# Kernel optimization log

Hardware: AMD Instinct MI355X
Metric: run time of the kernel (lower is better)

The kernel has to match this reference:

```python
import jax, jax.numpy as jnp
import numpy as np
import math

N_NODES = 10000
N_EDGES = 30000
N_FEAT = 128
N_GRAPHS = 50
HEADS = 8
OUT_DIM = 10


def _lin_params(key, fin, fout):
    kw, kb = jax.random.split(key)
    s = 1.0 / math.sqrt(fin)
    w = jax.random.uniform(kw, (fin, fout), jnp.float32, -s, s)
    b = jax.random.uniform(kb, (fout,), jnp.float32, -s, s)
    return w, b


def setup_inputs() -> dict:
    key = jax.random.key(0)
    ks = jax.random.split(key, 20)
    inp = {}
    inp["x"] = jax.random.normal(ks[0], (N_NODES, N_FEAT), jnp.float32)
    inp["edge_index"] = jax.random.randint(ks[1], (2, N_EDGES), 0, N_NODES)
    inp["batch"] = jnp.sort(jax.random.randint(ks[2], (N_NODES,), 0, N_GRAPHS))
    # (fin, out_channels) per layer; internal width = out_channels * HEADS
    dims = [(128, 512), (512, 256), (256, 64)]
    ki = 3
    for i, (fin, cout) in enumerate(dims, 1):
        hc = cout * HEADS
        inp[f"q{i}_w"], inp[f"q{i}_b"] = _lin_params(ks[ki], fin, hc); ki += 1
        inp[f"k{i}_w"], inp[f"k{i}_b"] = _lin_params(ks[ki], fin, hc); ki += 1
        inp[f"v{i}_w"], inp[f"v{i}_b"] = _lin_params(ks[ki], fin, hc); ki += 1
        inp[f"s{i}_w"], inp[f"s{i}_b"] = _lin_params(ks[ki], fin, cout); ki += 1
    inp["gate_w"], inp["gate_b"] = _lin_params(ks[ki], 64, 1); ki += 1
    inp["fc_w"], inp["fc_b"] = _lin_params(ks[ki], 64, OUT_DIM)
    return inp


def _tconv(x, src, dst, qw, qb, kw_, kb_, vw, vb, sw, sb):
    # PyG TransformerConv, heads=HEADS, concat=False (mean over heads), root_weight=True
    N = x.shape[0]
    hc = qw.shape[1]
    C = hc // HEADS
    q = (x @ qw + qb).reshape(N, HEADS, C)
    k = (x @ kw_ + kb_).reshape(N, HEADS, C)
    v = (x @ vw + vb).reshape(N, HEADS, C)
    # per-edge attention logits [E, H]
    alpha = (q[dst] * k[src]).sum(-1) * (1.0 / math.sqrt(C))
    # segment softmax over incoming edges of each destination node
    m = jax.ops.segment_max(alpha, dst, num_segments=N)
    ex = jnp.exp(alpha - m[dst])
    den = jax.ops.segment_sum(ex, dst, num_segments=N)
    w = ex / jnp.maximum(den[dst], 1e-16)
    agg = jax.ops.segment_sum(w[:, :, None] * v[src], dst, num_segments=N)  # [N,H,C]
    return agg.mean(axis=1) + x @ sw + sb


def reference(x, edge_index, batch,
              q1_w, q1_b, k1_w, k1_b, v1_w, v1_b, s1_w, s1_b,
              q2_w, q2_b, k2_w, k2_b, v2_w, v2_b, s2_w, s2_b,
              q3_w, q3_b, k3_w, k3_b, v3_w, v3_b, s3_w, s3_b,
              gate_w, gate_b, fc_w, fc_b):
    src, dst = edge_index[0], edge_index[1]
    h = jax.nn.elu(_tconv(x, src, dst, q1_w, q1_b, k1_w, k1_b, v1_w, v1_b, s1_w, s1_b))
    h = jax.nn.elu(_tconv(h, src, dst, q2_w, q2_b, k2_w, k2_b, v2_w, v2_b, s2_w, s2_b))
    h = jax.nn.elu(_tconv(h, src, dst, q3_w, q3_b, k3_w, k3_b, v3_w, v3_b, s3_w, s3_b))
    # GlobalAttention pooling: softmax(gate) within each graph, weighted sum
    gate = h @ gate_w + gate_b  # [N,1]
    gm = jax.ops.segment_max(gate, batch, num_segments=N_GRAPHS)
    ge = jnp.exp(gate - gm[batch])
    gd = jax.ops.segment_sum(ge, batch, num_segments=N_GRAPHS)
    g = ge / jnp.maximum(gd[batch], 1e-16)
    pooled = jax.ops.segment_sum(g * h, batch, num_segments=N_GRAPHS)  # [G,64]
    return pooled @ fc_w + fc_b
```

## Files before the change

### kernel.cpp

```cpp
#include <hip/hip_runtime.h>
#include <stdint.h>
#include <math.h>

#define NN 10000
#define NE 30000
#define NG 50
#define NH 8

typedef _Float16 f16;
typedef _Float16 f16x2 __attribute__((ext_vector_type(2)));
typedef _Float16 f16x4 __attribute__((ext_vector_type(4)));
typedef _Float16 f16x8 __attribute__((ext_vector_type(8)));
typedef float f32x4 __attribute__((ext_vector_type(4)));

__device__ inline void async16(f16* l, const f16* g) {
    __builtin_amdgcn_global_load_lds((const __attribute__((address_space(1))) void*)g,
                                     (__attribute__((address_space(3))) void*)l, 16, 0, 0);
}

__global__ __launch_bounds__(1024) void csr_build(const int* __restrict__ src, const int* __restrict__ dst,
                                                  const int* __restrict__ batch,
                                                  int* __restrict__ offs, int* __restrict__ srcCSR,
                                                  int* __restrict__ goffs) {
    __shared__ int cnt[NN];
    __shared__ int tot[1024];
    const int t = threadIdx.x;

    for (int i = t; i < NN; i += 1024) cnt[i] = 0;
    __syncthreads();
    for (int e = t; e < NE; e += 1024) atomicAdd(&cnt[dst[e]], 1);
    __syncthreads();

    const int base = t * 10;
    int v[10];
    int s = 0;
#pragma unroll
    for (int i = 0; i < 10; ++i) {
        int idx = base + i;
        v[i] = (idx < NN) ? cnt[idx] : 0;
        s += v[i];
    }
    tot[t] = s;
    __syncthreads();
    for (int d2 = 1; d2 < 1024; d2 <<= 1) {
        int add = (t >= d2) ? tot[t - d2] : 0;
        __syncthreads();
        tot[t] += add;
        __syncthreads();
    }
    int run = tot[t] - s;
    if (t == 0) offs[0] = 0;
    int curs[10];
#pragma unroll
    for (int i = 0; i < 10; ++i) {
        int idx = base + i;
        curs[i] = run;
        run += v[i];
        if (idx < NN) offs[idx + 1] = run;
    }
    __syncthreads();
#pragma unroll
    for (int i = 0; i < 10; ++i) {
        int idx = base + i;
        if (idx < NN) cnt[idx] = curs[i];
    }
    __syncthreads();

    for (int e = t; e < NE; e += 1024) {
        int p = atomicAdd(&cnt[dst[e]], 1);
        srcCSR[p] = src[e];
    }
    __syncthreads();

    for (int n = t; n < NN; n += 1024) {
        int s0 = offs[n], e0 = offs[n + 1];
        for (int i = s0 + 1; i < e0; ++i) {
            int vv = srcCSR[i];
            int j = i - 1;
            while (j >= s0 && srcCSR[j] > vv) { srcCSR[j + 1] = srcCSR[j]; --j; }
            srcCSR[j + 1] = vv;
        }
    }

    if (t <= NG) {
        int lo = 0, hi = NN;
        while (lo < hi) {
            int mid = (lo + hi) >> 1;
            if (batch[mid] < t) lo = mid + 1; else hi = mid;
        }
        goffs[t] = lo;
    }
}

#define MB_CVTX   0
#define MB_CVTQ   5000
#define MB_CVTK   7048
#define MB_P4L2   9096
#define MB_P4L3   9896
#define MB_PZB    10000
#define MB_PU     10296
#define MB_ZERO   10808
#define MB_TOTAL  10815

__device__ void prep4_tile(const float* __restrict__ W0, int n0, const float* __restrict__ W1, int n1,
                           const float* __restrict__ W2, int n2, const float* __restrict__ W3, int n3,
                           const float* __restrict__ b0, const float* __restrict__ b1,
                           const float* __restrict__ b2, const float* __restrict__ b3,
                           f16* __restrict__ Bt, float* __restrict__ bias, int K, int bx, int by) {
    __shared__ float tile[64][65];
    const int k0 = bx * 64;
    const int nb = by * 64;
    const int tid = threadIdx.x;
    const int tn = tid & 63;
    const int t4 = tid >> 6;
#pragma unroll
    for (int i = 0; i < 16; ++i) {
        int kl = t4 + i * 4;
        int k = k0 + kl;
        int n = nb + tn;
        float w = 0.0f;
        int m = n;
        if (m < n0) w = W0[(size_t)k * n0 + m];
        else { m -= n0;
            if (m < n1) w = W1[(size_t)k * n1 + m];
            else { m -= n1;
                if (m < n2) w = W2[(size_t)k * n2 + m];
                else { m -= n2; if (m < n3) w = W3[(size_t)k * n3 + m]; }
            }
        }
        tile[kl][tn] = w;
    }
    if (bx == 0 && t4 == 0) {
        int n = nb + tn;
        float bv = 0.0f;
        int m = n;
        if (m < n0) bv = b0[m];
        else { m -= n0;
            if (m < n1) bv = b1[m];
            else { m -= n1;
                if (m < n2) bv = b2[m];
                else { m -= n2; if (m < n3) bv = b3[m]; }
            }
        }
        bias[n] = bv;
    }
    __syncthreads();
#pragma unroll
    for (int i = 0; i < 16; ++i) {
        int nl = t4 + i * 4;
        Bt[(size_t)(nb + nl) * K + k0 + tn] = (f16)tile[tn][nl];
    }
}

__global__ __launch_bounds__(256) void megaprep(
        const float* __restrict__ x, f16* __restrict__ xh,
        const float* __restrict__ qw1, f16* __restrict__ qw16,
        const float* __restrict__ kw1, f16* __restrict__ kw16,
        const float* __restrict__ qb1, const float* __restrict__ kb1,
        const float* __restrict__ vw1, const float* __restrict__ sw1,
        const float* __restrict__ vb1, const float* __restrict__ sb1,
        const float* __restrict__ qw2, const float* __restrict__ qb2,
        const float* __restrict__ kw2, const float* __restrict__ kb2,
        const float* __restrict__ vw2, const float* __restrict__ vb2,
        const float* __restrict__ sw2, const float* __restrict__ sb2,
        const float* __restrict__ qw3, const float* __restrict__ qb3,
        const float* __restrict__ kw3, const float* __restrict__ kb3,
        const float* __restrict__ vw3, const float* __restrict__ vb3,
        const float* __restrict__ sw3, const float* __restrict__ sb3,
        f16* __restrict__ BtL2, float* __restrict__ biasL2,
        f16* __restrict__ BtL3, float* __restrict__ biasL3,
        f16* __restrict__ BtZ, float* __restrict__ biasZ,
        f16* __restrict__ BtY, float* __restrict__ biasY,
        float* __restrict__ zbias) {
    const int b = blockIdx.x;
    const int tid = threadIdx.x;

    if (b < MB_CVTQ) {
        int i = b * 256 + tid;
        if (i < NN * 128) xh[i] = (f16)x[i];
    } else if (b < MB_CVTK) {
        int i = (b - MB_CVTQ) * 256 + tid;
        qw16[i] = (f16)qw1[i];
    } else if (b < MB_P4L2) {
        int i = (b - MB_CVTK) * 256 + tid;
        kw16[i] = (f16)kw1[i];
    } else if (b < MB_P4L3) {
        int r = b - MB_P4L2;
        prep4_tile(qw2, 2048, kw2, 2048, vw2, 2048, sw2, 256,
                   qb2, kb2, vb2, sb2, BtL2, biasL2, 512, r & 7, r >> 3);
    } else if (b < MB_PZB) {
        int r = b - MB_P4L3;
        prep4_tile(qw3, 512, kw3, 512, vw3, 512, sw3, 64,
                   qb3, kb3, vb3, sb3, BtL3, biasL3, 256, r & 3, r >> 2);
    } else if (b < MB_PU) {
        int r = b - MB_PZB;
        int bx = r % 37, by = r / 37;
        __shared__ f16 ztile[32][65];
        const int k0 = bx * 32, c0 = by * 64;
#pragma unroll
        for (int i = 0; i < 8; ++i) {
            int idx = tid + i * 256;
            int kl = idx >> 6, cl = idx & 63;
            int k = k0 + kl, c = c0 + cl;
            float v = 0.0f;
            if (k < 1024)      v = vw1[(size_t)(k & 127) * 4096 + (k >> 7) * 512 + c];
            else if (k < 1152) v = sw1[(size_t)(k - 1024) * 512 + c];
            else if (k < 1160) v = vb1[(k - 1152) * 512 + c];
            ztile[kl][cl] = (f16)v;
        }
        if (bx == 0 && tid < 64) biasZ[c0 + tid] = sb1[c0 + tid];
        __syncthreads();
        const int cl = tid >> 2, kl = (tid & 3) * 8;
        f16x8 v;
#pragma unroll
        for (int t2 = 0; t2 < 8; ++t2) v[t2] = ztile[kl + t2][cl];
        *(f16x8*)(BtZ + (size_t)(c0 + cl) * 1184 + k0 + kl) = v;
    } else if (b < MB_ZERO) {
        const int fin = 128, hc = 4096, C = 512;
        const int wid = (b - MB_PU) * 4 + (tid >> 6);
        const int lane = tid & 63;
        if (wid >= fin * 16) return;
        const int k = wid >> 4;
        const int idx = wid & 15;
        const int h = idx & 7, isV = idx >> 3;
        const float* W = isV ? kw1 : qw1;
        const float* bvec = isV ? qb1 : kb1;
        float s = 0.0f;
        for (int c = lane; c < C; c += 64) s += W[(size_t)k * hc + h * C + c] * bvec[h * C + c];
#pragma unroll
        for (int o = 32; o > 0; o >>= 1) s += __shfl_down(s, o, 64);
        if (lane == 0) BtY[(size_t)(8 * fin + isV * 8 + h) * fin + k] = (f16)s;
        if (wid < 8) {
            float cc = 0.0f;
            for (int c = lane; c < C; c += 64) cc += qb1[wid * C + c] * kb1[wid * C + c];
#pragma unroll
            for (int o = 32; o > 0; o >>= 1) cc += __shfl_down(cc, o, 64);
            if (lane == 0) biasY[8 * fin + wid] = cc;
        }
    } else {
        int idx = (b - MB_ZERO) * 256 + tid;
        if (idx < 512) zbias[idx] = 0.0f;
        else if (idx < 1536) biasY[idx - 512] = 0.0f;
        else if (idx < 1656) biasY[1032 + idx - 1536] = 0.0f;
    }
}

__global__ __launch_bounds__(256) void gemm128(const f16* __restrict__ A, int lda, int zA,
                                               const f16* __restrict__ Bt, int ldb, int zB,
                                               const float* __restrict__ bias,
                                               f16* __restrict__ C, int ldc, int zC,
                                               float* __restrict__ Sf,
                                               int M, int Np, int K, int hcS, int Sw, int act) {
    __shared__ f16 smem[24576];
    const int rm = blockIdx.x * 128;
    if (rm >= M) return;
    A  += (size_t)blockIdx.z * zA;
    Bt += (size_t)blockIdx.z * zB;
    C  += (size_t)blockIdx.z * zC;
    const int tid  = threadIdx.x;
    const int lane = tid & 63;
    const int wave = tid >> 6;
    const int l16  = lane & 15;
    const int quad = lane >> 4;
    const int cn   = blockIdx.y * 128;
    const int wrow = (wave >> 1) * 64;
    const int wcol = (wave & 1) * 64;

    const int rS  = tid >> 2;
    const int kc  = ((tid & 3) ^ ((tid >> 3) & 3)) << 3;
    int rowA0 = rm + rS;       if (rowA0 >= M) rowA0 = M - 1;
    int rowA1 = rm + rS + 64;  if (rowA1 >= M) rowA1 = M - 1;
    const f16* gA0 = A + (size_t)rowA0 * lda + kc;
    const f16* gA1 = A + (size_t)rowA1 * lda + kc;
    const f16* gB0 = Bt + (size_t)(cn + rS) * ldb + kc;
    const f16* gB1 = Bt + (size_t)(cn + rS + 64) * ldb + kc;

    const int swf = (l16 >> 1) & 3;
    const int rdAoff = (wrow + l16) * 32 + ((quad ^ swf) << 3);
    const int rdBoff = 4096 + (wcol + l16) * 32 + ((quad ^ swf) << 3);

    f32x4 acc[4][4] = {};

    auto stage_load = [&](int slot) {
        f16* base = smem + slot * 8192;
        async16(base + tid * 8, gA0);
        async16(base + tid * 8 + 2048, gA1);
        async16(base + 4096 + tid * 8, gB0);
        async16(base + 4096 + tid * 8 + 2048, gB1);
        gA0 += 32; gA1 += 32; gB0 += 32; gB1 += 32;
    };

    const int NI = K >> 5;
    stage_load(0);
    stage_load(1);

    int slot = 0;
    for (int i = 0; i < NI; ++i) {
        if (i + 1 < NI) asm volatile("s_waitcnt vmcnt(4)" ::: "memory");
        else            asm volatile("s_waitcnt vmcnt(0)" ::: "memory");
        asm volatile("s_barrier" ::: "memory");
        if (i + 2 < NI) {
            int s2 = slot + 2; if (s2 >= 3) s2 -= 3;
            stage_load(s2);
        }
        const f16* sb = smem + slot * 8192;
        f16x8 av[4], bv[4];
#pragma unroll
        for (int ii = 0; ii < 4; ++ii) av[ii] = *(const f16x8*)(sb + rdAoff + ii * 512);
#pragma unroll
        for (int j = 0; j < 4; ++j) bv[j] = *(const f16x8*)(sb + rdBoff + j * 512);
#pragma unroll
        for (int ii = 0; ii < 4; ++ii)
#pragma unroll
            for (int j = 0; j < 4; ++j)
                acc[ii][j] = __builtin_amdgcn_mfma_f32_16x16x32_f16(bv[j], av[ii], acc[ii][j], 0, 0, 0);
        ++slot; if (slot == 3) slot = 0;
    }
    __syncthreads();

    f16* sC = smem;
    for (int round = 0; round < 2; ++round) {
        if ((wave >> 1) == round) {
#pragma unroll
            for (int j = 0; j < 4; ++j) {
                const int cb = wcol + j * 16 + quad * 4;
                const float4 bb = *(const float4*)(bias + cn + cb);
#pragma unroll
                for (int i = 0; i < 4; ++i) {
                    const int r = i * 16 + l16;
                    float v0 = acc[i][j][0] + bb.x;
                    float v1 = acc[i][j][1] + bb.y;
                    float v2 = acc[i][j][2] + bb.z;
                    float v3 = acc[i][j][3] + bb.w;
                    if (act) {
                        v0 = v0 > 0.0f ? v0 : (__expf(v0) - 1.0f);
                        v1 = v1 > 0.0f ? v1 : (__expf(v1) - 1.0f);
                        v2 = v2 > 0.0f ? v2 : (__expf(v2) - 1.0f);
                        v3 = v3 > 0.0f ? v3 : (__expf(v3) - 1.0f);
                    }
                    f16x4 o;
                    o[0] = (f16)v0; o[1] = (f16)v1; o[2] = (f16)v2; o[3] = (f16)v3;
                    *(f16x4*)(sC + r * 136 + cb) = o;
                    if (Sf) {
                        const int sc = cn + cb - hcS;
                        if (sc >= 0 && sc < Sw) {
                            const int grow = rm + round * 64 + r;
                            if (grow < M) {
                                float4 sv = { v0, v1, v2, v3 };
                                *(float4*)(Sf + (size_t)grow * Sw + sc) = sv;
                            }
                        }
                    }
                }
            }
        }
        __syncthreads();
#pragma unroll
        for (int it = 0; it < 4; ++it) {
            const int r = it * 16 + (tid >> 4);
            const int ch = tid & 15;
            const int grow = rm + round * 64 + r;
            if (grow < M) {
                f16x8 v = *(const f16x8*)(sC + r * 136 + ch * 8);
                *(f16x8*)(C + (size_t)grow * ldc + cn + ch * 8) = v;
            }
        }
        __syncthreads();
    }
}

__global__ __launch_bounds__(256) void alpha_zagg(const f16* __restrict__ Y, const f16* __restrict__ X,
                                                  const int* __restrict__ offs,
                                                  const int* __restrict__ srcCSR,
                                                  f16* __restrict__ Z,
                                                  int strideY, float scale) {
    const int fin = 128;
    const int n = blockIdx.x;
    const int e0 = offs[n];
    int d = offs[n + 1] - e0;
    if (d > 256) d = 256;

    __shared__ __align__(16) f16 sy[1024];
    __shared__ float sew[256 * NH];
    __shared__ float sv[256 * NH];
    __shared__ int sed[256];
    __shared__ float su[NH];
    __shared__ __align__(16) f16 sx[32 * 128];
    const int tid = threadIdx.x;

    const f16* Yn = Y + (size_t)n * strideY;
    for (int c = tid; c < fin; c += 256) ((f16x8*)sy)[c] = ((const f16x8*)Yn)[c];
    if (tid < NH) su[tid] = (float)Yn[8 * fin + tid];
    for (int e = tid; e < d; e += 256) {
        int s = srcCSR[e0 + e];
        sed[e] = s;
        f16x8 vv = *(const f16x8*)(Y + (size_t)s * strideY + 8 * fin + 8);
#pragma unroll
        for (int t = 0; t < 8; ++t) sv[e * NH + t] = (float)vv[t];
    }
    __syncthreads();

    {
        const int wv = tid >> 6, lane = tid & 63;
        for (int e = wv; e < d; e += 4) {
            const f16x8* kg = (const f16x8*)(X + (size_t)sed[e] * fin);
#pragma unroll
            for (int p = 0; p < 2; ++p) {
                const int ci = p * 64 + lane;
                const int head = ci >> 4;
                const int kcn = ci & 15;
                f16x8 yv = ((const f16x8*)sy)[ci];
                f16x8 xv = kg[kcn];
                float acc = 0.0f;
#pragma unroll
                for (int t = 0; t < 8; ++t) acc += (float)yv[t] * (float)xv[t];
#pragma unroll
                for (int o = 8; o > 0; o >>= 1) acc += __shfl_down(acc, o, 16);
                if ((lane & 15) == 0)
                    sew[e * NH + head] = (acc + su[head] + sv[e * NH + head]) * scale;
            }
        }
    }
    __syncthreads();

    if (tid < NH) {
        const int h = tid;
        float m = -3.0e38f;
        for (int e = 0; e < d; ++e) m = fmaxf(m, sew[e * NH + h]);
        float den = 0.0f;
        for (int e = 0; e < d; ++e) {
            float ex = __expf(sew[e * NH + h] - m);
            sew[e * NH + h] = ex;
            den += ex;
        }
        float inv = 1.0f / (fmaxf(den, 1e-16f) * (float)NH);
        for (int e = 0; e < d; ++e) sew[e * NH + h] *= inv;
    }
    __syncthreads();

    const int h = tid >> 5;
    const int f0 = (tid * 4) & 127;
    float a0 = 0.0f, a1 = 0.0f, a2 = 0.0f, a3 = 0.0f;
    for (int ch = 0; ch < d; ch += 32) {
        const int cnt = min(32, d - ch);
        for (int idx = tid; idx < cnt * 16; idx += 256) {
            int row = idx >> 4, c8 = idx & 15;
            *(f16x8*)(sx + row * 128 + c8 * 8) = *(const f16x8*)(X + (size_t)sed[ch + row] * 128 + c8 * 8);
        }
        __syncthreads();
        for (int e = 0; e < cnt; ++e) {
            float w = sew[(ch + e) * NH + h];
            f16x4 xv = *(const f16x4*)(sx + e * 128 + f0);
            a0 += w * (float)xv[0];
            a1 += w * (float)xv[1];
            a2 += w * (float)xv[2];
            a3 += w * (float)xv[3];
        }
        __syncthreads();
    }
    f16* Zr = Z + (size_t)n * 1184;
    f16x4 o; o[0] = (f16)a0; o[1] = (f16)a1; o[2] = (f16)a2; o[3] = (f16)a3;
    *(f16x4*)(Zr + tid * 4) = o;
    if (tid < 16) *(f16x8*)(Zr + 1024 + tid * 8) = *(const f16x8*)(X + (size_t)n * 128 + tid * 8);
    if (tid >= 32 && tid < 40) {
        int hh = tid - 32;
        float s = 0.0f;
        for (int e = 0; e < d; ++e) s += sew[e * NH + hh];
        Zr[1152 + hh] = (f16)s;
    }
    if (tid >= 64 && tid < 88) Zr[1160 + (tid - 64)] = (f16)0.0f;
}

__global__ __launch_bounds__(256) void edge_node(const f16* __restrict__ QKVS,
                                                 const float* __restrict__ Sf,
                                                 const int* __restrict__ offs,
                                                 const int* __restrict__ srcCSR,
                                                 float* __restrict__ hout, f16* __restrict__ houth,
                                                 int Np, int C, int hc, float scale, int writeHout) {
    const int n = blockIdx.x;
    const int e0 = offs[n];
    int d = offs[n + 1] - e0;
    if (d > 256) d = 256;

    __shared__ __align__(16) f16 sq[4096];
    __shared__ float sew[256 * NH];
    __shared__ int sed[256];
    __shared__ float sred[512];
    const int tid = threadIdx.x;

    const f16x8* qg = (const f16x8*)(QKVS + (size_t)n * Np);
    const int qchunks = hc >> 3;
    for (int c = tid; c < qchunks; c += 256) ((f16x8*)sq)[c] = qg[c];
    for (int e = tid; e < d; e += 256) sed[e] = srcCSR[e0 + e];
    __syncthreads();

    {
        const int wv = tid >> 6, lane = tid & 63;
        const int cph = C >> 3;
        const int passes = (hc >> 9) ? (hc >> 9) : 1;
        for (int e = wv; e < d; e += 4) {
            const f16x8* kg = (const f16x8*)(QKVS + (size_t)sed[e] * Np + hc);
            for (int p = 0; p < passes; ++p) {
                const int ci = p * 64 + lane;
                f16x8 qv = ((const f16x8*)sq)[ci];
                f16x8 kv = kg[ci];
                float acc = 0.0f;
#pragma unroll
                for (int t = 0; t < 8; ++t) acc += (float)qv[t] * (float)kv[t];
                for (int o = cph >> 1; o > 0; o >>= 1) acc += __shfl_down(acc, o, cph);
                if ((lane & (cph - 1)) == 0) {
                    const int head = ci / cph;
                    sew[e * NH + head] = acc * scale;
                }
            }
        }
    }
    __syncthreads();

    if (tid < NH) {
        const int h = tid;
        float m = -3.0e38f;
        for (int e = 0; e < d; ++e) m = fmaxf(m, sew[e * NH + h]);
        float den = 0.0f;
        for (int e = 0; e < d; ++e) {
            float ex = __expf(sew[e * NH + h] - m);
            sew[e * NH + h] = ex;
            den += ex;
        }
        float inv = 1.0f / (fmaxf(den, 1e-16f) * (float)NH);
        for (int e = 0; e < d; ++e) sew[e * NH + h] *= inv;
    }
    __syncthreads();

    const int half = C >> 1;
    const int cp = tid & (half - 1);
    const int grp = tid / half;
    const int ngr = 256 / half;
    float a0 = 0.0f, a1 = 0.0f;
    for (int e = grp; e < d; e += ngr) {
        const unsigned int* vp = (const unsigned int*)(QKVS + (size_t)sed[e] * Np + 2 * hc);
#pragma unroll
        for (int h = 0; h < NH; ++h) {
            float w = sew[e * NH + h];
            f16x2 vv = __builtin_bit_cast(f16x2, vp[((h * C) >> 1) + cp]);
            a0 += w * (float)vv.x;
            a1 += w * (float)vv.y;
        }
    }
    if (ngr > 1) {
        sred[tid] = a0;
        sred[256 + tid] = a1;
        __syncthreads();
        if (grp == 0) {
            for (int g = 1; g < ngr; ++g) {
                a0 += sred[g * half + cp];
                a1 += sred[256 + g * half + cp];
            }
        }
    }
    if (grp == 0) {
        const int c = cp * 2;
        const float* Sp = Sf + (size_t)n * C;
        float o0 = a0 + Sp[c];
        float o1 = a1 + Sp[c + 1];
        o0 = o0 > 0.0f ? o0 : (__expf(o0) - 1.0f);
        o1 = o1 > 0.0f ? o1 : (__expf(o1) - 1.0f);
        if (writeHout) {
            hout[(size_t)n * C + c] = o0;
            hout[(size_t)n * C + c + 1] = o1;
        }
        houth[(size_t)n * C + c] = (f16)o0;
        houth[(size_t)n * C + c + 1] = (f16)o1;
    }
}

__global__ __launch_bounds__(256) void pool_graph(const float* __restrict__ h,
                                                  const float* __restrict__ gw, const float* __restrict__ gb,
                                                  const float* __restrict__ fcw, const float* __restrict__ fcb,
                                                  const int* __restrict__ goffs,
                                                  float* __restrict__ gbuf, float* __restrict__ out) {
    const int g = blockIdx.x;
    const int s = goffs[g], e = goffs[g + 1];
    const int tid = threadIdx.x;
    const int wv = tid >> 6, lane = tid & 63;

    __shared__ float red[256];
    __shared__ float pl[64];
    __shared__ float sden;

    if (e == s) {
        if (tid < 10) out[g * 10 + tid] = fcb[tid];
        return;
    }

    const float gwl = gw[lane];
    for (int n = s + wv; n < e; n += 4) {
        float acc = h[(size_t)n * 64 + lane] * gwl;
#pragma unroll
        for (int o = 32; o > 0; o >>= 1) acc += __shfl_down(acc, o, 64);
        if (lane == 0) gbuf[n] = acc + gb[0];
    }
    __syncthreads();

    float m = -3.0e38f;
    for (int n = s + tid; n < e; n += 256) m = fmaxf(m, gbuf[n]);
    red[tid] = m;
    __syncthreads();
    for (int o = 128; o > 0; o >>= 1) {
        if (tid < o) red[tid] = fmaxf(red[tid], red[tid + o]);
        __syncthreads();
    }
    m = red[0];
    __syncthreads();

    float sum = 0.0f;
    for (int n = s + tid; n < e; n += 256) {
        float ex = __expf(gbuf[n] - m);
        gbuf[n] = ex;
        sum += ex;
    }
    red[tid] = sum;
    __syncthreads();
    for (int o = 128; o > 0; o >>= 1) {
        if (tid < o) red[tid] += red[tid + o];
        __syncthreads();
    }
    if (tid == 0) sden = 1.0f / fmaxf(red[0], 1e-16f);
    __syncthreads();

    float acc = 0.0f;
    for (int n = s + wv; n < e; n += 4) acc += gbuf[n] * h[(size_t)n * 64 + lane];
    red[tid] = acc;
    __syncthreads();
    if (wv == 0) pl[lane] = (red[lane] + red[64 + lane] + red[128 + lane] + red[192 + lane]) * sden;
    __syncthreads();

    if (tid < 10) {
        float o = fcb[tid];
#pragma unroll
        for (int c = 0; c < 64; ++c) o += pl[c] * fcw[c * 10 + tid];
        out[g * 10 + tid] = o;
    }
}

extern "C" void kernel_launch(void* const* d_in, const int* in_sizes, int n_in,
                              void* d_out, int out_size, void* d_ws, size_t ws_size,
                              hipStream_t stream) {
    const float* x   = (const float*)d_in[0];
    const int* ei    = (const int*)d_in[1];
    const int* src   = ei;
    const int* dst   = ei + NE;
    const int* batch = (const int*)d_in[2];

    struct LayerW { int fin, C, hc; const float *qw,*qb,*kw,*kb,*vw,*vb,*sw,*sb; };
    LayerW LW[3];
    const int fins[3] = {128, 512, 256};
    const int Cs[3]   = {512, 256, 64};
    for (int l = 0; l < 3; ++l) {
        int b = 3 + 8 * l;
        LW[l].fin = fins[l]; LW[l].C = Cs[l]; LW[l].hc = Cs[l] * NH;
        LW[l].qw = (const float*)d_in[b + 0]; LW[l].qb = (const float*)d_in[b + 1];
        LW[l].kw = (const float*)d_in[b + 2]; LW[l].kb = (const float*)d_in[b + 3];
        LW[l].vw = (const float*)d_in[b + 4]; LW[l].vb = (const float*)d_in[b + 5];
        LW[l].sw = (const float*)d_in[b + 6]; LW[l].sb = (const float*)d_in[b + 7];
    }
    const float* gate_w = (const float*)d_in[27];
    const float* gate_b = (const float*)d_in[28];
    const float* fc_w   = (const float*)d_in[29];
    const float* fc_b   = (const float*)d_in[30];

    size_t off = 0;
    char* ws = (char*)d_ws;
    auto alloc = [&](size_t bytes) -> void* {
        void* p = ws + off;
        off = (off + bytes + 255) & ~(size_t)255;
        return p;
    };
    f16* BtL2   = (f16*)alloc((size_t)6400 * 512 * sizeof(f16));
    f16* BtL3   = (f16*)alloc((size_t)1664 * 256 * sizeof(f16));
    f16* BtZ    = (f16*)alloc((size_t)512 * 1184 * sizeof(f16));
    float* biasL2 = (float*)alloc(6400 * sizeof(float));
    float* biasL3 = (float*)alloc(1664 * sizeof(float));
    float* biasZ  = (float*)alloc(512 * sizeof(float));
    f16* QKbuf  = (f16*)alloc((size_t)NN * 6400 * sizeof(f16));
    f16* Zbuf   = (f16*)alloc((size_t)NN * 1184 * sizeof(f16));
    float* Sf   = (float*)alloc((size_t)NN * 256 * sizeof(float));
    f16* xh     = (f16*)alloc((size_t)NN * 128 * sizeof(f16));
    f16* houth  = (f16*)alloc((size_t)NN * 512 * sizeof(f16));
    float* hf   = (float*)alloc((size_t)NN * 64 * sizeof(float));
    f16* qw16   = (f16*)alloc((size_t)128 * 4096 * sizeof(f16));
    f16* kw16   = (f16*)alloc((size_t)128 * 4096 * sizeof(f16));
    f16* BtY    = (f16*)alloc((size_t)1152 * 128 * sizeof(f16));
    float* zbias = (float*)alloc(512 * sizeof(float));
    float* biasY = (float*)alloc(1152 * sizeof(float));
    int* offs   = (int*)alloc((NN + 1) * sizeof(int));
    int* srcCSR = (int*)alloc(NE * sizeof(int));
    int* goffs  = (int*)alloc((NG + 1) * sizeof(int));
    float* gbuf = (float*)alloc(NN * sizeof(float));
    if (off > ws_size) return;

    megaprep<<<MB_TOTAL, 256, 0, stream>>>(
        x, xh, LW[0].qw, qw16, LW[0].kw, kw16,
        LW[0].qb, LW[0].kb, LW[0].vw, LW[0].sw, LW[0].vb, LW[0].sb,
        LW[1].qw, LW[1].qb, LW[1].kw, LW[1].kb, LW[1].vw, LW[1].vb, LW[1].sw, LW[1].sb,
        LW[2].qw, LW[2].qb, LW[2].kw, LW[2].kb, LW[2].vw, LW[2].vb, LW[2].sw, LW[2].sb,
        BtL2, biasL2, BtL3, biasL3, BtZ, biasZ, BtY, biasY, zbias);

    csr_build<<<1, 1024, 0, stream>>>(src, dst, batch, offs, srcCSR, goffs);

    const int grid_m = 80;

    {
        const int fin = 128, hc = 4096, NtotY = 1152;
        const float scale = 1.0f / sqrtf(512.0f);
        dim3 gm(1, 1, 8);
        gemm128<<<gm, 256, 0, stream>>>(kw16, hc, 512, qw16, hc, 512, zbias,
                                        BtY, fin, fin * fin, nullptr, fin, fin, 512, 0, 0, 0);
        dim3 gy(grid_m, NtotY / 128);
        gemm128<<<gy, 256, 0, stream>>>(xh, fin, 0, BtY, fin, 0, biasY,
                                        QKbuf, NtotY, 0, nullptr, NN, NtotY, fin, 0, 0, 0);
        alpha_zagg<<<NN, 256, 0, stream>>>(QKbuf, xh, offs, srcCSR, Zbuf, NtotY, scale);
        dim3 gz(grid_m, 4);
        gemm128<<<gz, 256, 0, stream>>>(Zbuf, 1184, 0, BtZ, 1184, 0, biasZ,
                                        houth, 512, 0, nullptr, NN, 512, 1184, 0, 0, 1);
    }
    const f16* Acur = houth;
    for (int l = 1; l < 3; ++l) {
        const int K = LW[l].fin, C = LW[l].C, hc = LW[l].hc;
        const float scale = 1.0f / sqrtf((float)C);
        const int Np = (3 * hc + C + 127) & ~127;
        f16* Bt = (l == 1) ? BtL2 : BtL3;
        float* bias = (l == 1) ? biasL2 : biasL3;
        dim3 gq(grid_m, Np / 128);
        gemm128<<<gq, 256, 0, stream>>>(Acur, K, 0, Bt, K, 0, bias,
                                        QKbuf, Np, 0, Sf, NN, Np, K, 3 * hc, C, 0);
        edge_node<<<NN, 256, 0, stream>>>(QKbuf, Sf, offs, srcCSR, hf, houth,
                                          Np, C, hc, scale, l == 2 ? 1 : 0);
        Acur = houth;
    }

    pool_graph<<<NG, 256, 0, stream>>>(hf, gate_w, gate_b, fc_w, fc_b, goffs, gbuf, (float*)d_out);
}
```

Measured before the change: 561.4 us.

## Split single-block CSR build into multi-block histogram, scan, scatter, sort kernels

```diff
diff --git a/kernel.cpp b/kernel.cpp
--- a/kernel.cpp
+++ b/kernel.cpp
@@ -18,26 +18,34 @@
                                      (__attribute__((address_space(3))) void*)l, 16, 0, 0);
 }
 
-__global__ __launch_bounds__(1024) void csr_build(const int* __restrict__ src, const int* __restrict__ dst,
-                                                  const int* __restrict__ batch,
-                                                  int* __restrict__ offs, int* __restrict__ srcCSR,
-                                                  int* __restrict__ goffs) {
-    __shared__ int cnt[NN];
+__global__ void hist_kernel(const int* __restrict__ dst, int* __restrict__ deg, int E) {
+    int e = blockIdx.x * blockDim.x + threadIdx.x;
+    if (e < E) atomicAdd(&deg[dst[e]], 1);
+}
+
+__global__ __launch_bounds__(1024) void scan_goffs(const int* __restrict__ deg, int* __restrict__ offs,
+                                                   int* __restrict__ cursor,
+                                                   const int* __restrict__ batch, int* __restrict__ goffs) {
+    if (blockIdx.x == 1) {
+        int g = threadIdx.x;
+        if (g > NG) return;
+        int lo = 0, hi = NN;
+        while (lo < hi) {
+            int mid = (lo + hi) >> 1;
+            if (batch[mid] < g) lo = mid + 1; else hi = mid;
+        }
+        goffs[g] = lo;
+        return;
+    }
     __shared__ int tot[1024];
     const int t = threadIdx.x;
-
-    for (int i = t; i < NN; i += 1024) cnt[i] = 0;
-    __syncthreads();
-    for (int e = t; e < NE; e += 1024) atomicAdd(&cnt[dst[e]], 1);
-    __syncthreads();
-
     const int base = t * 10;
     int v[10];
     int s = 0;
 #pragma unroll
     for (int i = 0; i < 10; ++i) {
         int idx = base + i;
-        v[i] = (idx < NN) ? cnt[idx] : 0;
+        v[i] = (idx < NN) ? deg[idx] : 0;
         s += v[i];
     }
     tot[t] = s;
@@ -50,45 +58,33 @@
     }
     int run = tot[t] - s;
     if (t == 0) offs[0] = 0;
-    int curs[10];
 #pragma unroll
     for (int i = 0; i < 10; ++i) {
         int idx = base + i;
-        curs[i] = run;
+        if (idx < NN) cursor[idx] = run;
         run += v[i];
         if (idx < NN) offs[idx + 1] = run;
     }
-    __syncthreads();
-#pragma unroll
-    for (int i = 0; i < 10; ++i) {
-        int idx = base + i;
-        if (idx < NN) cnt[idx] = curs[i];
-    }
-    __syncthreads();
-
-    for (int e = t; e < NE; e += 1024) {
-        int p = atomicAdd(&cnt[dst[e]], 1);
+}
+
+__global__ void scatter_kernel(const int* __restrict__ src, const int* __restrict__ dst,
+                               int* __restrict__ cursor, int* __restrict__ srcCSR, int E) {
+    int e = blockIdx.x * blockDim.x + threadIdx.x;
+    if (e < E) {
+        int p = atomicAdd(&cursor[dst[e]], 1);
         srcCSR[p] = src[e];
     }
-    __syncthreads();
-
-    for (int n = t; n < NN; n += 1024) {
-        int s0 = offs[n], e0 = offs[n + 1];
-        for (int i = s0 + 1; i < e0; ++i) {
-            int vv = srcCSR[i];
-            int j = i - 1;
-            while (j >= s0 && srcCSR[j] > vv) { srcCSR[j + 1] = srcCSR[j]; --j; }
-            srcCSR[j + 1] = vv;
-        }
-    }
-
-    if (t <= NG) {
-        int lo = 0, hi = NN;
-        while (lo < hi) {
-            int mid = (lo + hi) >> 1;
-            if (batch[mid] < t) lo = mid + 1; else hi = mid;
-        }
-        goffs[t] = lo;
+}
+
+__global__ void sort_csr(const int* __restrict__ offs, int* __restrict__ srcCSR) {
+    int n = blockIdx.x * blockDim.x + threadIdx.x;
+    if (n >= NN) return;
+    int s = offs[n], e = offs[n + 1];
+    for (int i = s + 1; i < e; ++i) {
+        int v = srcCSR[i];
+        int j = i - 1;
+        while (j >= s && srcCSR[j] > v) { srcCSR[j + 1] = srcCSR[j]; --j; }
+        srcCSR[j + 1] = v;
     }
 }
 
@@ -100,7 +96,7 @@
 #define MB_PZB    10000
 #define MB_PU     10296
 #define MB_ZERO   10808
-#define MB_TOTAL  10815
+#define MB_TOTAL  10854
 
 __device__ void prep4_tile(const float* __restrict__ W0, int n0, const float* __restrict__ W1, int n1,
                            const float* __restrict__ W2, int n2, const float* __restrict__ W3, int n3,
@@ -171,7 +167,7 @@
         f16* __restrict__ BtL3, float* __restrict__ biasL3,
         f16* __restrict__ BtZ, float* __restrict__ biasZ,
         f16* __restrict__ BtY, float* __restrict__ biasY,
-        float* __restrict__ zbias) {
+        float* __restrict__ zbias, int* __restrict__ deg) {
     const int b = blockIdx.x;
     const int tid = threadIdx.x;
 
@@ -242,6 +238,7 @@
         if (idx < 512) zbias[idx] = 0.0f;
         else if (idx < 1536) biasY[idx - 512] = 0.0f;
         else if (idx < 1656) biasY[1032 + idx - 1536] = 0.0f;
+        else if (idx < 1656 + NN) deg[idx - 1656] = 0;
     }
 }
 
@@ -693,7 +690,9 @@
     f16* BtY    = (f16*)alloc((size_t)1152 * 128 * sizeof(f16));
     float* zbias = (float*)alloc(512 * sizeof(float));
     float* biasY = (float*)alloc(1152 * sizeof(float));
+    int* deg    = (int*)alloc(NN * sizeof(int));
     int* offs   = (int*)alloc((NN + 1) * sizeof(int));
+    int* cursor = (int*)alloc(NN * sizeof(int));
     int* srcCSR = (int*)alloc(NE * sizeof(int));
     int* goffs  = (int*)alloc((NG + 1) * sizeof(int));
     float* gbuf = (float*)alloc(NN * sizeof(float));
@@ -704,9 +703,12 @@
         LW[0].qb, LW[0].kb, LW[0].vw, LW[0].sw, LW[0].vb, LW[0].sb,
         LW[1].qw, LW[1].qb, LW[1].kw, LW[1].kb, LW[1].vw, LW[1].vb, LW[1].sw, LW[1].sb,
         LW[2].qw, LW[2].qb, LW[2].kw, LW[2].kb, LW[2].vw, LW[2].vb, LW[2].sw, LW[2].sb,
-        BtL2, biasL2, BtL3, biasL3, BtZ, biasZ, BtY, biasY, zbias);
-
-    csr_build<<<1, 1024, 0, stream>>>(src, dst, batch, offs, srcCSR, goffs);
+        BtL2, biasL2, BtL3, biasL3, BtZ, biasZ, BtY, biasY, zbias, deg);
+
+    hist_kernel<<<(NE + 255) / 256, 256, 0, stream>>>(dst, deg, NE);
+    scan_goffs<<<2, 1024, 0, stream>>>(deg, offs, cursor, batch, goffs);
+    scatter_kernel<<<(NE + 255) / 256, 256, 0, stream>>>(src, dst, cursor, srcCSR, NE);
+    sort_csr<<<(NN + 255) / 256, 256, 0, stream>>>(offs, srcCSR);
 
     const int grid_m = 80;
 
```

Result: faster. 462.3 us (median of 2 runs) (-17.6%).
